# Performance work log

Hardware: AMD Instinct MI355X
Metric: run time of the kernel (lower is better)

## Reference

```python
import jax, jax.numpy as jnp
import numpy as np

N_NODES = 100000
N_EDGES = 1600000
IN_DIM, HID_DIM, OUT_DIM = 128, 64, 64
NEG_SLOPE = 0.2


def _gat_layer(h_in, src, dst, W, a_src, a_dst, b, n_nodes):
    # h: [N, F_out]
    h = h_in @ W.T
    alpha_src = h @ a_src  # [N]
    alpha_dst = h @ a_dst  # [N]
    # per-edge raw attention logits (edge j->i: src=j, dst=i)
    e = jax.nn.leaky_relu(alpha_src[src] + alpha_dst[dst], NEG_SLOPE)  # [E]
    # segment softmax over incoming edges of each dst node
    m = jax.ops.segment_max(e, dst, num_segments=n_nodes)
    ex = jnp.exp(e - m[dst])
    denom = jax.ops.segment_sum(ex, dst, num_segments=n_nodes)
    alpha = ex / denom[dst]  # [E], denom > 0 thanks to self-loops
    out = jax.ops.segment_sum(h[src] * alpha[:, None], dst, num_segments=n_nodes)
    return out + b


def setup_inputs() -> dict:
    key = jax.random.key(0)
    ks = jax.random.split(key, 12)
    x = jax.random.normal(ks[0], (N_NODES, IN_DIM), dtype=jnp.float32)
    edge_index = jax.random.randint(ks[1], (2, N_EDGES), 0, N_NODES)
    edge_attr = jax.random.normal(ks[2], (N_EDGES, 1), dtype=jnp.float32)
    s1 = 1.0 / np.sqrt(IN_DIM)
    s2 = 1.0 / np.sqrt(HID_DIM)
    W1 = jax.random.normal(ks[3], (HID_DIM, IN_DIM), dtype=jnp.float32) * s1
    att_src1 = jax.random.normal(ks[4], (HID_DIM,), dtype=jnp.float32) * s2
    att_dst1 = jax.random.normal(ks[5], (HID_DIM,), dtype=jnp.float32) * s2
    b1 = jnp.zeros((HID_DIM,), dtype=jnp.float32)
    W2 = jax.random.normal(ks[6], (OUT_DIM, HID_DIM), dtype=jnp.float32) * s2
    att_src2 = jax.random.normal(ks[7], (OUT_DIM,), dtype=jnp.float32) * s2
    att_dst2 = jax.random.normal(ks[8], (OUT_DIM,), dtype=jnp.float32) * s2
    b2 = jnp.zeros((OUT_DIM,), dtype=jnp.float32)
    return {"x": x, "edge_index": edge_index, "edge_attr": edge_attr,
            "W1": W1, "att_src1": att_src1, "att_dst1": att_dst1, "b1": b1,
            "W2": W2, "att_src2": att_src2, "att_dst2": att_dst2, "b2": b2}


def reference(x, edge_index, edge_attr, W1, att_src1, att_dst1, b1,
              W2, att_src2, att_dst2, b2):
    n = x.shape[0]
    # add self-loops (PyG GATConv default); edge_attr unused (edge_dim=None)
    loop = jnp.arange(n, dtype=edge_index.dtype)
    src = jnp.concatenate([edge_index[0], loop])
    dst = jnp.concatenate([edge_index[1], loop])
    h = _gat_layer(x, src, dst, W1, att_src1, att_dst1, b1, n)
    h = jax.nn.relu(h)
    h = _gat_layer(h, src, dst, W2, att_src2, att_dst2, b2, n)
    # global_mean_pool with batch=None -> mean over all nodes, shape [1, F]
    return jnp.mean(h, axis=0, keepdims=True)
```

## Files before the change

kernel.cpp:

```cpp
#include <hip/hip_runtime.h>

#define NEG_SLOPE 0.2f
#define BSHIFT 6
#define NBMAX 2048
#define BCAP 1408
#define CHUNK 4096

typedef __attribute__((ext_vector_type(8))) short short8;
typedef __attribute__((ext_vector_type(4))) float f32x4;

__device__ __forceinline__ unsigned short f2b(float x) {
    unsigned u = __float_as_uint(x);
    u += 0x7fff + ((u >> 16) & 1);
    return (unsigned short)(u >> 16);
}
__device__ __forceinline__ float b2f(unsigned short u) {
    return __uint_as_float((unsigned)u << 16);
}

__global__ __launch_bounds__(256) void hist_kernel(
    const int* __restrict__ ei, int* __restrict__ hist, int E, int NB)
{
    __shared__ int cnt[NBMAX];
    const int tid = threadIdx.x;
    for (int i = tid; i < NB; i += 256) cnt[i] = 0;
    __syncthreads();
    const int start = blockIdx.x * CHUNK;
    const int end = min(start + CHUNK, E);
    for (int i = start + tid; i < end; i += 256)
        atomicAdd(&cnt[ei[E + i] >> BSHIFT], 1);
    __syncthreads();
    for (int i = tid; i < NB; i += 256)
        hist[(size_t)blockIdx.x * NB + i] = cnt[i];
}

__global__ __launch_bounds__(256) void colscan_kernel(
    int* __restrict__ hist, int* __restrict__ btotal, int NB, int NBLK)
{
    const int b = blockIdx.x * 256 + threadIdx.x;
    if (b >= NB) return;
    int run = 0;
    int blk = 0;
    for (; blk + 8 <= NBLK; blk += 8) {
        int w[8];
        #pragma unroll
        for (int j = 0; j < 8; ++j) w[j] = hist[(size_t)(blk + j) * NB + b];
        #pragma unroll
        for (int j = 0; j < 8; ++j) {
            hist[(size_t)(blk + j) * NB + b] = run;
            run += w[j];
        }
    }
    for (; blk < NBLK; ++blk) {
        int w = hist[(size_t)blk * NB + b];
        hist[(size_t)blk * NB + b] = run;
        run += w;
    }
    btotal[b] = run;
}

__global__ __launch_bounds__(256) void scatter_kernel(
    const int* __restrict__ ei, const int* __restrict__ hist,
    int* __restrict__ binned, int E, int NB)
{
    __shared__ int base[NBMAX], cnt2[NBMAX];
    const int tid = threadIdx.x;
    for (int i = tid; i < NB; i += 256) {
        base[i] = hist[(size_t)blockIdx.x * NB + i];
        cnt2[i] = 0;
    }
    __syncthreads();
    const int start = blockIdx.x * CHUNK;
    const int end = min(start + CHUNK, E);
    for (int i = start + tid; i < end; i += 256) {
        int s = ei[i], d = ei[E + i];
        int b = d >> BSHIFT;
        int r = base[b] + atomicAdd(&cnt2[b], 1);
        if (r < BCAP) binned[(size_t)b * BCAP + r] = (s << BSHIFT) | (d & 63);
    }
}

__global__ __launch_bounds__(256) void bscan_kernel(
    const int* __restrict__ btotal, int* __restrict__ bbase, int NB)
{
    __shared__ int lds[256];
    const int t = threadIdx.x;
    int v[8]; int s = 0;
    #pragma unroll
    for (int j = 0; j < 8; ++j) {
        int i = t * 8 + j;
        v[j] = (i < NB) ? min(btotal[i], BCAP) : 0;
        s += v[j];
    }
    lds[t] = s;
    __syncthreads();
    #pragma unroll
    for (int off = 1; off < 256; off <<= 1) {
        int x = (t >= off) ? lds[t - off] : 0;
        __syncthreads();
        lds[t] += x;
        __syncthreads();
    }
    int excl = (t > 0) ? lds[t - 1] : 0;
    #pragma unroll
    for (int j = 0; j < 8; ++j) {
        int i = t * 8 + j;
        if (i < NB) { bbase[i] = excl + 64 * i; excl += v[j]; }
    }
}

__global__ __launch_bounds__(256) void bucket_csr_kernel(
    const int* __restrict__ binned, const int* __restrict__ btotal,
    const int* __restrict__ bbase, int* __restrict__ row_ptr,
    int* __restrict__ esrc, int N)
{
    __shared__ int ldeg[64];
    __shared__ int lcur[64];
    const int b = blockIdx.x;
    const int tid = threadIdx.x;
    const int node0 = b << BSHIFT;
    const int cnt = min(btotal[b], BCAP);
    const int base_e = bbase[b];
    const int* bp = binned + (size_t)b * BCAP;

    if (tid < 64) ldeg[tid] = (node0 + tid < N) ? 1 : 0;
    __syncthreads();
    for (int i = tid; i < cnt; i += 256)
        atomicAdd(&ldeg[bp[i] & 63], 1);
    __syncthreads();
    if (tid < 64) {
        int v = ldeg[tid];
        int inc = v;
        #pragma unroll
        for (int off = 1; off < 64; off <<= 1) {
            int t2 = __shfl_up(inc, off, 64);
            if (tid >= off) inc += t2;
        }
        int excl = inc - v;
        int node = node0 + tid;
        if (node <= N) row_ptr[node] = base_e + excl;
        if (node < N) {
            esrc[base_e + excl] = node;
            lcur[tid] = base_e + excl + 1;
        }
    }
    __syncthreads();
    for (int i = tid; i < cnt; i += 256) {
        int v = bp[i];
        int pos = atomicAdd(&lcur[v & 63], 1);
        esrc[pos] = v >> BSHIFT;
    }
}

template<int K, bool BF16IN>
__global__ __launch_bounds__(256) void gemm_attn_kernel(
    const void* __restrict__ in_v, const float* __restrict__ W,
    const float* __restrict__ a_src, const float* __restrict__ a_dst,
    unsigned short* __restrict__ hb, float* __restrict__ asrc,
    float* __restrict__ adst, int N)
{
    constexpr int LDK = K + 8;
    __shared__ unsigned short xb[64 * LDK];
    __shared__ unsigned short wb[64 * LDK];
    __shared__ float avs[64], avd[64];

    const int tid = threadIdx.x;
    const int node0 = blockIdx.x * 64;
    const int w = tid >> 6;
    const int lane = tid & 63;
    const int col = lane & 15;
    const int quad = lane >> 4;

    if (tid < 64) { avs[tid] = a_src[tid]; avd[tid] = a_dst[tid]; }

    for (int i = tid; i < 64 * (K / 4); i += 256) {
        int r = i / (K / 4), c = i % (K / 4);
        float4 v = *(const float4*)&W[(size_t)r * K + 4 * c];
        *(ushort4*)&wb[r * LDK + 4 * c] =
            make_ushort4(f2b(v.x), f2b(v.y), f2b(v.z), f2b(v.w));
    }
    if (BF16IN) {
        const unsigned short* in = (const unsigned short*)in_v;
        for (int i = tid; i < 64 * (K / 8); i += 256) {
            int r = i / (K / 8), c = i % (K / 8);
            int node = node0 + r;
            ulonglong2 v = (node < N)
                ? *(const ulonglong2*)&in[(size_t)node * K + 8 * c]
                : make_ulonglong2(0ull, 0ull);
            *(ulonglong2*)&xb[r * LDK + 8 * c] = v;
        }
    } else {
        const float* in = (const float*)in_v;
        for (int i = tid; i < 64 * (K / 4); i += 256) {
            int r = i / (K / 4), c = i % (K / 4);
            int node = node0 + r;
            float4 v = (node < N) ? *(const float4*)&in[(size_t)node * K + 4 * c]
                                  : make_float4(0.f, 0.f, 0.f, 0.f);
            *(ushort4*)&xb[r * LDK + 4 * c] =
                make_ushort4(f2b(v.x), f2b(v.y), f2b(v.z), f2b(v.w));
        }
    }
    __syncthreads();

    f32x4 acc[4] = {f32x4{0,0,0,0}, f32x4{0,0,0,0}, f32x4{0,0,0,0}, f32x4{0,0,0,0}};
    #pragma unroll
    for (int kc = 0; kc < K / 32; ++kc) {
        short8 a = *(const short8*)&xb[(16 * w + col) * LDK + kc * 32 + quad * 8];
        #pragma unroll
        for (int j = 0; j < 4; ++j) {
            short8 b = *(const short8*)&wb[(16 * j + col) * LDK + kc * 32 + quad * 8];
            acc[j] = __builtin_amdgcn_mfma_f32_16x16x32_bf16(a, b, acc[j], 0, 0, 0);
        }
    }

    #pragma unroll
    for (int r = 0; r < 4; ++r) {
        const int node = node0 + 16 * w + quad * 4 + r;
        const bool valid = node < N;
        float vs = 0.f, vd = 0.f;
        #pragma unroll
        for (int j = 0; j < 4; ++j) {
            float hv = acc[j][r];
            int f = 16 * j + col;
            if (valid) hb[(size_t)node * 64 + f] = f2b(hv);
            vs = fmaf(hv, avs[f], vs);
            vd = fmaf(hv, avd[f], vd);
        }
        #pragma unroll
        for (int off = 8; off >= 1; off >>= 1) {
            vs += __shfl_down(vs, off, 16);
            vd += __shfl_down(vd, off, 16);
        }
        if (col == 0 && valid) { asrc[node] = vs; adst[node] = vd; }
    }
}

__global__ __launch_bounds__(256) void aggregate_csr_kernel(
    const int* __restrict__ row_ptr, const int* __restrict__ esrc,
    const float* __restrict__ asrc, const float* __restrict__ adst,
    const unsigned short* __restrict__ hb, const float* __restrict__ bias,
    unsigned short* __restrict__ gb, int N, int do_relu)
{
    const int node = (int)((blockIdx.x * 256 + threadIdx.x) >> 4);
    const int lane = threadIdx.x & 15;
    if (node >= N) return;
    const int beg = row_ptr[node];
    const int end = row_ptr[node + 1];
    const float ad = adst[node];
    float a0 = 0.f, a1 = 0.f, a2 = 0.f, a3 = 0.f, wsum = 0.f;
    int p = beg;
    for (; p + 4 <= end; p += 4) {
        int s[4]; ushort4 r[4]; float l[4];
        #pragma unroll
        for (int j = 0; j < 4; ++j) s[j] = esrc[p + j];
        #pragma unroll
        for (int j = 0; j < 4; ++j)
            r[j] = *(const ushort4*)(hb + (size_t)s[j] * 64 + lane * 4);
        #pragma unroll
        for (int j = 0; j < 4; ++j) l[j] = asrc[s[j]] + ad;
        #pragma unroll
        for (int j = 0; j < 4; ++j) {
            float ll = (l[j] > 0.f) ? l[j] : NEG_SLOPE * l[j];
            float w = __expf(ll);
            wsum += w;
            a0 = fmaf(w, b2f(r[j].x), a0);
            a1 = fmaf(w, b2f(r[j].y), a1);
            a2 = fmaf(w, b2f(r[j].z), a2);
            a3 = fmaf(w, b2f(r[j].w), a3);
        }
    }
    for (; p < end; ++p) {
        int s = esrc[p];
        ushort4 r = *(const ushort4*)(hb + (size_t)s * 64 + lane * 4);
        float l = asrc[s] + ad;
        l = (l > 0.f) ? l : NEG_SLOPE * l;
        float w = __expf(l);
        wsum += w;
        a0 = fmaf(w, b2f(r.x), a0);
        a1 = fmaf(w, b2f(r.y), a1);
        a2 = fmaf(w, b2f(r.z), a2);
        a3 = fmaf(w, b2f(r.w), a3);
    }
    const float inv = 1.0f / wsum;
    float4 v = make_float4(a0 * inv, a1 * inv, a2 * inv, a3 * inv);
    if (bias) {
        v.x += bias[lane * 4 + 0]; v.y += bias[lane * 4 + 1];
        v.z += bias[lane * 4 + 2]; v.w += bias[lane * 4 + 3];
    }
    if (do_relu) {
        v.x = fmaxf(v.x, 0.f); v.y = fmaxf(v.y, 0.f);
        v.z = fmaxf(v.z, 0.f); v.w = fmaxf(v.w, 0.f);
    }
    *(ushort4*)&gb[(size_t)node * 64 + lane * 4] =
        make_ushort4(f2b(v.x), f2b(v.y), f2b(v.z), f2b(v.w));
}

__global__ __launch_bounds__(256) void pool_kernel(
    const unsigned short* __restrict__ gb, const float* __restrict__ b2,
    float* __restrict__ out, int N)
{
    __shared__ float red[256];
    const int f = threadIdx.x & 63;
    const int sub = threadIdx.x >> 6;
    float acc = 0.f;
    for (int n = blockIdx.x * 4 + sub; n < N; n += gridDim.x * 4)
        acc += b2f(gb[(size_t)n * 64 + f]);
    red[threadIdx.x] = acc;
    __syncthreads();
    if (threadIdx.x < 64) {
        float s = red[f] + red[64 + f] + red[128 + f] + red[192 + f];
        atomicAdd(out + f, s * (1.0f / (float)N));
        if (blockIdx.x == 0) atomicAdd(out + f, b2[f]);
    }
}

extern "C" void kernel_launch(void* const* d_in, const int* in_sizes, int n_in,
                              void* d_out, int out_size, void* d_ws, size_t ws_size,
                              hipStream_t stream) {
    const float* x   = (const float*)d_in[0];
    const int*   ei  = (const int*)d_in[1];
    const float* W1  = (const float*)d_in[3];
    const float* as1 = (const float*)d_in[4];
    const float* ad1 = (const float*)d_in[5];
    const float* b1  = (const float*)d_in[6];
    const float* W2  = (const float*)d_in[7];
    const float* as2 = (const float*)d_in[8];
    const float* ad2 = (const float*)d_in[9];
    const float* b2  = (const float*)d_in[10];
    float* out = (float*)d_out;

    const int N = in_sizes[0] / 128;
    const int E = in_sizes[1] / 2;
    const int Etot = E + N;
    const int NB = (N + 63) >> BSHIFT;
    const int NBLK = (E + CHUNK - 1) / CHUNK;

    auto align4 = [](size_t v) { return (v + 3) & ~(size_t)3; };
    float* ws    = (float*)d_ws;
    size_t off = 0;
    unsigned short* hb = (unsigned short*)(ws + off); off += align4((size_t)N * 32);
    unsigned short* gb = (unsigned short*)(ws + off); off += align4((size_t)N * 32);
    float* asrc  = ws + off; off += align4(N);
    float* adst  = ws + off; off += align4(N);
    int* row_ptr = (int*)(ws + off); off += align4(N + 1);
    int* btotal  = (int*)(ws + off); off += NBMAX;
    int* bbase   = (int*)(ws + off); off += NBMAX;
    int* hist    = (int*)(ws + off); off += align4((size_t)NBLK * NB);
    int* esrc    = (int*)(ws + off); off += align4(Etot);
    int* binned  = (int*)gb;

    const int gemm_blocks = (N + 63) / 64;
    const int agg_blocks  = (int)(((size_t)N * 16 + 255) / 256);

    hipMemsetAsync(out, 0, 64 * sizeof(float), stream);

    hist_kernel<<<NBLK, 256, 0, stream>>>(ei, hist, E, NB);
    colscan_kernel<<<(NB + 255) / 256, 256, 0, stream>>>(hist, btotal, NB, NBLK);
    scatter_kernel<<<NBLK, 256, 0, stream>>>(ei, hist, binned, E, NB);
    bscan_kernel<<<1, 256, 0, stream>>>(btotal, bbase, NB);
    bucket_csr_kernel<<<NB, 256, 0, stream>>>(binned, btotal, bbase, row_ptr, esrc, N);

    gemm_attn_kernel<128, false><<<gemm_blocks, 256, 0, stream>>>(
        x, W1, as1, ad1, hb, asrc, adst, N);
    aggregate_csr_kernel<<<agg_blocks, 256, 0, stream>>>(
        row_ptr, esrc, asrc, adst, hb, b1, gb, N, 1);

    gemm_attn_kernel<64, true><<<gemm_blocks, 256, 0, stream>>>(
        gb, W2, as2, ad2, hb, asrc, adst, N);
    aggregate_csr_kernel<<<agg_blocks, 256, 0, stream>>>(
        row_ptr, esrc, asrc, adst, hb, nullptr, gb, N, 0);

    pool_kernel<<<512, 256, 0, stream>>>(gb, b2, out, N);
}
```

Baseline: 301.8 us.

## Build CSR with global atomics and widen per-lane aggregation to 16 features

Replaces the bucketed histogram/scatter CSR construction with a per-node degree count using global atomics, a two-pass block scan, and a direct atomic-cursor scatter of source indices. It also drops the BCAP per-bucket truncation. Separately, the aggregation kernel now uses 4 lanes per node with 16 features each, loaded as two 16-byte vectors, instead of 16 lanes with 4 features. The CSR change trades shared-memory binning for contended global atomics and scattered writes. The aggregation change raises register use and lowers thread-level parallelism per node.

```diff
diff --git a/kernel.cpp b/kernel.cpp
--- a/kernel.cpp
+++ b/kernel.cpp
@@ -1,10 +1,6 @@
 #include <hip/hip_runtime.h>
 
 #define NEG_SLOPE 0.2f
-#define BSHIFT 6
-#define NBMAX 2048
-#define BCAP 1408
-#define CHUNK 4096
 
 typedef __attribute__((ext_vector_type(8))) short short8;
 typedef __attribute__((ext_vector_type(4))) float f32x4;
@@ -18,78 +14,27 @@
     return __uint_as_float((unsigned)u << 16);
 }
 
-__global__ __launch_bounds__(256) void hist_kernel(
-    const int* __restrict__ ei, int* __restrict__ hist, int E, int NB)
-{
-    __shared__ int cnt[NBMAX];
-    const int tid = threadIdx.x;
-    for (int i = tid; i < NB; i += 256) cnt[i] = 0;
-    __syncthreads();
-    const int start = blockIdx.x * CHUNK;
-    const int end = min(start + CHUNK, E);
-    for (int i = start + tid; i < end; i += 256)
-        atomicAdd(&cnt[ei[E + i] >> BSHIFT], 1);
-    __syncthreads();
-    for (int i = tid; i < NB; i += 256)
-        hist[(size_t)blockIdx.x * NB + i] = cnt[i];
-}
-
-__global__ __launch_bounds__(256) void colscan_kernel(
-    int* __restrict__ hist, int* __restrict__ btotal, int NB, int NBLK)
-{
-    const int b = blockIdx.x * 256 + threadIdx.x;
-    if (b >= NB) return;
-    int run = 0;
-    int blk = 0;
-    for (; blk + 8 <= NBLK; blk += 8) {
-        int w[8];
-        #pragma unroll
-        for (int j = 0; j < 8; ++j) w[j] = hist[(size_t)(blk + j) * NB + b];
-        #pragma unroll
-        for (int j = 0; j < 8; ++j) {
-            hist[(size_t)(blk + j) * NB + b] = run;
-            run += w[j];
-        }
-    }
-    for (; blk < NBLK; ++blk) {
-        int w = hist[(size_t)blk * NB + b];
-        hist[(size_t)blk * NB + b] = run;
-        run += w;
-    }
-    btotal[b] = run;
-}
-
-__global__ __launch_bounds__(256) void scatter_kernel(
-    const int* __restrict__ ei, const int* __restrict__ hist,
-    int* __restrict__ binned, int E, int NB)
-{
-    __shared__ int base[NBMAX], cnt2[NBMAX];
-    const int tid = threadIdx.x;
-    for (int i = tid; i < NB; i += 256) {
-        base[i] = hist[(size_t)blockIdx.x * NB + i];
-        cnt2[i] = 0;
-    }
-    __syncthreads();
-    const int start = blockIdx.x * CHUNK;
-    const int end = min(start + CHUNK, E);
-    for (int i = start + tid; i < end; i += 256) {
-        int s = ei[i], d = ei[E + i];
-        int b = d >> BSHIFT;
-        int r = base[b] + atomicAdd(&cnt2[b], 1);
-        if (r < BCAP) binned[(size_t)b * BCAP + r] = (s << BSHIFT) | (d & 63);
-    }
-}
-
-__global__ __launch_bounds__(256) void bscan_kernel(
-    const int* __restrict__ btotal, int* __restrict__ bbase, int NB)
+__global__ __launch_bounds__(256) void deg_kernel(
+    const int* __restrict__ ei, int* __restrict__ deg, int E)
+{
+    int i = blockIdx.x * 256 + threadIdx.x;
+    const int stride = gridDim.x * 256;
+    for (; i < E; i += stride)
+        atomicAdd(&deg[ei[E + i]], 1);
+}
+
+__global__ __launch_bounds__(256) void scan1_kernel(
+    const int* __restrict__ deg, int* __restrict__ row_ptr,
+    int* __restrict__ bsum, int N)
 {
     __shared__ int lds[256];
     const int t = threadIdx.x;
+    const int base = blockIdx.x * 2048 + t * 8;
     int v[8]; int s = 0;
     #pragma unroll
     for (int j = 0; j < 8; ++j) {
-        int i = t * 8 + j;
-        v[j] = (i < NB) ? min(btotal[i], BCAP) : 0;
+        int i = base + j;
+        v[j] = (i < N) ? deg[i] + 1 : 0;
         s += v[j];
     }
     lds[t] = s;
@@ -102,53 +47,48 @@
         __syncthreads();
     }
     int excl = (t > 0) ? lds[t - 1] : 0;
+    if (t == 255) bsum[blockIdx.x] = lds[255];
     #pragma unroll
     for (int j = 0; j < 8; ++j) {
-        int i = t * 8 + j;
-        if (i < NB) { bbase[i] = excl + 64 * i; excl += v[j]; }
-    }
-}
-
-__global__ __launch_bounds__(256) void bucket_csr_kernel(
-    const int* __restrict__ binned, const int* __restrict__ btotal,
-    const int* __restrict__ bbase, int* __restrict__ row_ptr,
-    int* __restrict__ esrc, int N)
-{
-    __shared__ int ldeg[64];
-    __shared__ int lcur[64];
-    const int b = blockIdx.x;
-    const int tid = threadIdx.x;
-    const int node0 = b << BSHIFT;
-    const int cnt = min(btotal[b], BCAP);
-    const int base_e = bbase[b];
-    const int* bp = binned + (size_t)b * BCAP;
-
-    if (tid < 64) ldeg[tid] = (node0 + tid < N) ? 1 : 0;
-    __syncthreads();
-    for (int i = tid; i < cnt; i += 256)
-        atomicAdd(&ldeg[bp[i] & 63], 1);
-    __syncthreads();
-    if (tid < 64) {
-        int v = ldeg[tid];
-        int inc = v;
-        #pragma unroll
-        for (int off = 1; off < 64; off <<= 1) {
-            int t2 = __shfl_up(inc, off, 64);
-            if (tid >= off) inc += t2;
-        }
-        int excl = inc - v;
-        int node = node0 + tid;
-        if (node <= N) row_ptr[node] = base_e + excl;
-        if (node < N) {
-            esrc[base_e + excl] = node;
-            lcur[tid] = base_e + excl + 1;
-        }
-    }
-    __syncthreads();
-    for (int i = tid; i < cnt; i += 256) {
-        int v = bp[i];
-        int pos = atomicAdd(&lcur[v & 63], 1);
-        esrc[pos] = v >> BSHIFT;
+        int i = base + j;
+        if (i < N) row_ptr[i] = excl;
+        excl += v[j];
+    }
+}
+
+__global__ __launch_bounds__(256) void scan2_kernel(
+    int* __restrict__ row_ptr, int* __restrict__ cursor,
+    int* __restrict__ esrc, const int* __restrict__ bsum, int N, int Etot)
+{
+    const int t = threadIdx.x;
+    const int blk = blockIdx.x;
+    int p = 0;
+    for (int j = 0; j < blk; ++j) p += bsum[j];
+    const int base = blk * 2048 + t * 8;
+    #pragma unroll
+    for (int j = 0; j < 8; ++j) {
+        int i = base + j;
+        if (i < N) {
+            int r = row_ptr[i] + p;
+            row_ptr[i] = r;
+            esrc[r] = i;
+            cursor[i] = r + 1;
+        }
+    }
+    if (blk == 0 && t == 0) row_ptr[N] = Etot;
+}
+
+__global__ __launch_bounds__(256) void scatter_direct_kernel(
+    const int* __restrict__ ei, int* __restrict__ cursor,
+    int* __restrict__ esrc, int E)
+{
+    int i = blockIdx.x * 256 + threadIdx.x;
+    const int stride = gridDim.x * 256;
+    for (; i < E; i += stride) {
+        int s = ei[i];
+        int d = ei[E + i];
+        int pos = atomicAdd(&cursor[d], 1);
+        esrc[pos] = s;
     }
 }
 
@@ -241,21 +181,30 @@
     const unsigned short* __restrict__ hb, const float* __restrict__ bias,
     unsigned short* __restrict__ gb, int N, int do_relu)
 {
-    const int node = (int)((blockIdx.x * 256 + threadIdx.x) >> 4);
-    const int lane = threadIdx.x & 15;
+    const int node = (int)((blockIdx.x * 256 + threadIdx.x) >> 2);
+    const int lane = threadIdx.x & 3;
     if (node >= N) return;
     const int beg = row_ptr[node];
     const int end = row_ptr[node + 1];
     const float ad = adst[node];
-    float a0 = 0.f, a1 = 0.f, a2 = 0.f, a3 = 0.f, wsum = 0.f;
+    const unsigned short* hbase = hb + lane * 16;
+
+    float acc[16];
+    #pragma unroll
+    for (int k = 0; k < 16; ++k) acc[k] = 0.f;
+    float wsum = 0.f;
+
     int p = beg;
     for (; p + 4 <= end; p += 4) {
-        int s[4]; ushort4 r[4]; float l[4];
+        int s[4]; short8 r0[4], r1[4]; float l[4];
         #pragma unroll
         for (int j = 0; j < 4; ++j) s[j] = esrc[p + j];
         #pragma unroll
-        for (int j = 0; j < 4; ++j)
-            r[j] = *(const ushort4*)(hb + (size_t)s[j] * 64 + lane * 4);
+        for (int j = 0; j < 4; ++j) {
+            const unsigned short* hp = hbase + (size_t)s[j] * 64;
+            r0[j] = *(const short8*)hp;
+            r1[j] = *(const short8*)(hp + 8);
+        }
         #pragma unroll
         for (int j = 0; j < 4; ++j) l[j] = asrc[s[j]] + ad;
         #pragma unroll
@@ -263,36 +212,45 @@
             float ll = (l[j] > 0.f) ? l[j] : NEG_SLOPE * l[j];
             float w = __expf(ll);
             wsum += w;
-            a0 = fmaf(w, b2f(r[j].x), a0);
-            a1 = fmaf(w, b2f(r[j].y), a1);
-            a2 = fmaf(w, b2f(r[j].z), a2);
-            a3 = fmaf(w, b2f(r[j].w), a3);
+            #pragma unroll
+            for (int k = 0; k < 8; ++k)
+                acc[k] = fmaf(w, b2f((unsigned short)r0[j][k]), acc[k]);
+            #pragma unroll
+            for (int k = 0; k < 8; ++k)
+                acc[8 + k] = fmaf(w, b2f((unsigned short)r1[j][k]), acc[8 + k]);
         }
     }
     for (; p < end; ++p) {
         int s = esrc[p];
-        ushort4 r = *(const ushort4*)(hb + (size_t)s * 64 + lane * 4);
+        const unsigned short* hp = hbase + (size_t)s * 64;
+        short8 r0 = *(const short8*)hp;
+        short8 r1 = *(const short8*)(hp + 8);
         float l = asrc[s] + ad;
         l = (l > 0.f) ? l : NEG_SLOPE * l;
         float w = __expf(l);
         wsum += w;
-        a0 = fmaf(w, b2f(r.x), a0);
-        a1 = fmaf(w, b2f(r.y), a1);
-        a2 = fmaf(w, b2f(r.z), a2);
-        a3 = fmaf(w, b2f(r.w), a3);
-    }
+        #pragma unroll
+        for (int k = 0; k < 8; ++k)
+            acc[k] = fmaf(w, b2f((unsigned short)r0[k]), acc[k]);
+        #pragma unroll
+        for (int k = 0; k < 8; ++k)
+            acc[8 + k] = fmaf(w, b2f((unsigned short)r1[k]), acc[8 + k]);
+    }
+
     const float inv = 1.0f / wsum;
-    float4 v = make_float4(a0 * inv, a1 * inv, a2 * inv, a3 * inv);
-    if (bias) {
-        v.x += bias[lane * 4 + 0]; v.y += bias[lane * 4 + 1];
-        v.z += bias[lane * 4 + 2]; v.w += bias[lane * 4 + 3];
-    }
-    if (do_relu) {
-        v.x = fmaxf(v.x, 0.f); v.y = fmaxf(v.y, 0.f);
-        v.z = fmaxf(v.z, 0.f); v.w = fmaxf(v.w, 0.f);
-    }
-    *(ushort4*)&gb[(size_t)node * 64 + lane * 4] =
-        make_ushort4(f2b(v.x), f2b(v.y), f2b(v.z), f2b(v.w));
+    short8 s0, s1;
+    #pragma unroll
+    for (int k = 0; k < 8; ++k) {
+        float v0 = acc[k] * inv;
+        float v1 = acc[8 + k] * inv;
+        if (bias) { v0 += bias[lane * 16 + k]; v1 += bias[lane * 16 + 8 + k]; }
+        if (do_relu) { v0 = fmaxf(v0, 0.f); v1 = fmaxf(v1, 0.f); }
+        s0[k] = (short)f2b(v0);
+        s1[k] = (short)f2b(v1);
+    }
+    unsigned short* gp = gb + (size_t)node * 64 + lane * 16;
+    *(short8*)gp = s0;
+    *(short8*)(gp + 8) = s1;
 }
 
 __global__ __launch_bounds__(256) void pool_kernel(
@@ -332,8 +290,6 @@
     const int N = in_sizes[0] / 128;
     const int E = in_sizes[1] / 2;
     const int Etot = E + N;
-    const int NB = (N + 63) >> BSHIFT;
-    const int NBLK = (E + CHUNK - 1) / CHUNK;
 
     auto align4 = [](size_t v) { return (v + 3) & ~(size_t)3; };
     float* ws    = (float*)d_ws;
@@ -343,22 +299,21 @@
     float* asrc  = ws + off; off += align4(N);
     float* adst  = ws + off; off += align4(N);
     int* row_ptr = (int*)(ws + off); off += align4(N + 1);
-    int* btotal  = (int*)(ws + off); off += NBMAX;
-    int* bbase   = (int*)(ws + off); off += NBMAX;
-    int* hist    = (int*)(ws + off); off += align4((size_t)NBLK * NB);
+    int* deg     = (int*)(ws + off); off += align4(N);
+    int* bsum    = (int*)(ws + off); off += 64;
     int* esrc    = (int*)(ws + off); off += align4(Etot);
-    int* binned  = (int*)gb;
 
     const int gemm_blocks = (N + 63) / 64;
-    const int agg_blocks  = (int)(((size_t)N * 16 + 255) / 256);
+    const int agg_blocks  = (int)(((size_t)N * 4 + 255) / 256);
+    const int NS1 = (N + 2047) / 2048;
 
     hipMemsetAsync(out, 0, 64 * sizeof(float), stream);
-
-    hist_kernel<<<NBLK, 256, 0, stream>>>(ei, hist, E, NB);
-    colscan_kernel<<<(NB + 255) / 256, 256, 0, stream>>>(hist, btotal, NB, NBLK);
-    scatter_kernel<<<NBLK, 256, 0, stream>>>(ei, hist, binned, E, NB);
-    bscan_kernel<<<1, 256, 0, stream>>>(btotal, bbase, NB);
-    bucket_csr_kernel<<<NB, 256, 0, stream>>>(binned, btotal, bbase, row_ptr, esrc, N);
+    hipMemsetAsync(deg, 0, (size_t)N * sizeof(int), stream);
+
+    deg_kernel<<<2048, 256, 0, stream>>>(ei, deg, E);
+    scan1_kernel<<<NS1, 256, 0, stream>>>(deg, row_ptr, bsum, N);
+    scan2_kernel<<<NS1, 256, 0, stream>>>(row_ptr, deg, esrc, bsum, N, Etot);
+    scatter_direct_kernel<<<2048, 256, 0, stream>>>(ei, deg, esrc, E);
 
     gemm_attn_kernel<128, false><<<gemm_blocks, 256, 0, stream>>>(
         x, W1, as1, ad1, hb, asrc, adst, N);
```

Result: slower. 448.4 us (+48.6%).

## Fuse final aggregation with mean pool, parallelize column scan, deepen gather unroll

Applied to the files above, without the earlier changes.

The second-layer aggregation now accumulates its normalized outputs straight into a shared-memory per-block sum and atomically adds to the pooled output. This removes the bf16 write of the final features and the separate pool kernel pass. The column scan uses one wavefront per bucket with a shuffle-based prefix scan instead of one serial thread per bucket. Scatter blocks are remapped to interleave chunk order, and the aggregation gather loop is unrolled to 8 edges to keep more loads in flight. The costs are more LDS atomics, higher register pressure from the deeper unroll, and a different float summation order in the pooled result.

```diff
diff --git a/kernel.cpp b/kernel.cpp
--- a/kernel.cpp
+++ b/kernel.cpp
@@ -37,26 +37,24 @@
 __global__ __launch_bounds__(256) void colscan_kernel(
     int* __restrict__ hist, int* __restrict__ btotal, int NB, int NBLK)
 {
-    const int b = blockIdx.x * 256 + threadIdx.x;
-    if (b >= NB) return;
+    const int col = (int)((blockIdx.x * 256 + threadIdx.x) >> 6);
+    const int ln  = threadIdx.x & 63;
+    if (col >= NB) return;
     int run = 0;
-    int blk = 0;
-    for (; blk + 8 <= NBLK; blk += 8) {
-        int w[8];
-        #pragma unroll
-        for (int j = 0; j < 8; ++j) w[j] = hist[(size_t)(blk + j) * NB + b];
-        #pragma unroll
-        for (int j = 0; j < 8; ++j) {
-            hist[(size_t)(blk + j) * NB + b] = run;
-            run += w[j];
-        }
-    }
-    for (; blk < NBLK; ++blk) {
-        int w = hist[(size_t)blk * NB + b];
-        hist[(size_t)blk * NB + b] = run;
-        run += w;
-    }
-    btotal[b] = run;
+    for (int r0 = 0; r0 < NBLK; r0 += 64) {
+        const int r = r0 + ln;
+        const bool ok = (r < NBLK);
+        int v = ok ? hist[(size_t)r * NB + col] : 0;
+        int inc = v;
+        #pragma unroll
+        for (int off = 1; off < 64; off <<= 1) {
+            int x = __shfl_up(inc, off, 64);
+            if (ln >= off) inc += x;
+        }
+        if (ok) hist[(size_t)r * NB + col] = run + inc - v;
+        run += __shfl(inc, 63, 64);
+    }
+    if (ln == 0) btotal[col] = run;
 }
 
 __global__ __launch_bounds__(256) void scatter_kernel(
@@ -64,13 +62,18 @@
     int* __restrict__ binned, int E, int NB)
 {
     __shared__ int base[NBMAX], cnt2[NBMAX];
+    const int nblk = gridDim.x;
+    const int q = nblk >> 3, rr = nblk & 7;
+    const int x = blockIdx.x & 7, k = blockIdx.x >> 3;
+    const int chunk = ((x < rr) ? x * (q + 1) : rr * (q + 1) + (x - rr) * q) + k;
+
     const int tid = threadIdx.x;
     for (int i = tid; i < NB; i += 256) {
-        base[i] = hist[(size_t)blockIdx.x * NB + i];
+        base[i] = hist[(size_t)chunk * NB + i];
         cnt2[i] = 0;
     }
     __syncthreads();
-    const int start = blockIdx.x * CHUNK;
+    const int start = chunk * CHUNK;
     const int end = min(start + CHUNK, E);
     for (int i = start + tid; i < end; i += 256) {
         int s = ei[i], d = ei[E + i];
@@ -249,17 +252,17 @@
     const float ad = adst[node];
     float a0 = 0.f, a1 = 0.f, a2 = 0.f, a3 = 0.f, wsum = 0.f;
     int p = beg;
-    for (; p + 4 <= end; p += 4) {
-        int s[4]; ushort4 r[4]; float l[4];
-        #pragma unroll
-        for (int j = 0; j < 4; ++j) s[j] = esrc[p + j];
-        #pragma unroll
-        for (int j = 0; j < 4; ++j)
+    for (; p + 8 <= end; p += 8) {
+        int s[8]; ushort4 r[8]; float l[8];
+        #pragma unroll
+        for (int j = 0; j < 8; ++j) s[j] = esrc[p + j];
+        #pragma unroll
+        for (int j = 0; j < 8; ++j)
             r[j] = *(const ushort4*)(hb + (size_t)s[j] * 64 + lane * 4);
         #pragma unroll
-        for (int j = 0; j < 4; ++j) l[j] = asrc[s[j]] + ad;
-        #pragma unroll
-        for (int j = 0; j < 4; ++j) {
+        for (int j = 0; j < 8; ++j) l[j] = asrc[s[j]] + ad;
+        #pragma unroll
+        for (int j = 0; j < 8; ++j) {
             float ll = (l[j] > 0.f) ? l[j] : NEG_SLOPE * l[j];
             float w = __expf(ll);
             wsum += w;
@@ -295,22 +298,70 @@
         make_ushort4(f2b(v.x), f2b(v.y), f2b(v.z), f2b(v.w));
 }
 
-__global__ __launch_bounds__(256) void pool_kernel(
-    const unsigned short* __restrict__ gb, const float* __restrict__ b2,
+__global__ __launch_bounds__(256) void aggregate_pool_kernel(
+    const int* __restrict__ row_ptr, const int* __restrict__ esrc,
+    const float* __restrict__ asrc, const float* __restrict__ adst,
+    const unsigned short* __restrict__ hb, const float* __restrict__ b2,
     float* __restrict__ out, int N)
 {
-    __shared__ float red[256];
-    const int f = threadIdx.x & 63;
-    const int sub = threadIdx.x >> 6;
-    float acc = 0.f;
-    for (int n = blockIdx.x * 4 + sub; n < N; n += gridDim.x * 4)
-        acc += b2f(gb[(size_t)n * 64 + f]);
-    red[threadIdx.x] = acc;
-    __syncthreads();
-    if (threadIdx.x < 64) {
-        float s = red[f] + red[64 + f] + red[128 + f] + red[192 + f];
-        atomicAdd(out + f, s * (1.0f / (float)N));
-        if (blockIdx.x == 0) atomicAdd(out + f, b2[f]);
+    __shared__ float red[64];
+    const int tid = threadIdx.x;
+    if (tid < 64) red[tid] = 0.f;
+    __syncthreads();
+
+    const int node = (int)((blockIdx.x * 256 + tid) >> 4);
+    const int lane = tid & 15;
+    const bool valid = node < N;
+    const int beg = valid ? row_ptr[node] : 0;
+    const int end = valid ? row_ptr[node + 1] : 0;
+    const float ad = valid ? adst[node] : 0.f;
+
+    float a0 = 0.f, a1 = 0.f, a2 = 0.f, a3 = 0.f, wsum = 0.f;
+    int p = beg;
+    for (; p + 8 <= end; p += 8) {
+        int s[8]; ushort4 r[8]; float l[8];
+        #pragma unroll
+        for (int j = 0; j < 8; ++j) s[j] = esrc[p + j];
+        #pragma unroll
+        for (int j = 0; j < 8; ++j)
+            r[j] = *(const ushort4*)(hb + (size_t)s[j] * 64 + lane * 4);
+        #pragma unroll
+        for (int j = 0; j < 8; ++j) l[j] = asrc[s[j]] + ad;
+        #pragma unroll
+        for (int j = 0; j < 8; ++j) {
+            float ll = (l[j] > 0.f) ? l[j] : NEG_SLOPE * l[j];
+            float w = __expf(ll);
+            wsum += w;
+            a0 = fmaf(w, b2f(r[j].x), a0);
+            a1 = fmaf(w, b2f(r[j].y), a1);
+            a2 = fmaf(w, b2f(r[j].z), a2);
+            a3 = fmaf(w, b2f(r[j].w), a3);
+        }
+    }
+    for (; p < end; ++p) {
+        int s = esrc[p];
+        ushort4 r = *(const ushort4*)(hb + (size_t)s * 64 + lane * 4);
+        float l = asrc[s] + ad;
+        l = (l > 0.f) ? l : NEG_SLOPE * l;
+        float w = __expf(l);
+        wsum += w;
+        a0 = fmaf(w, b2f(r.x), a0);
+        a1 = fmaf(w, b2f(r.y), a1);
+        a2 = fmaf(w, b2f(r.z), a2);
+        a3 = fmaf(w, b2f(r.w), a3);
+    }
+
+    if (valid) {
+        const float inv = 1.0f / wsum;
+        atomicAdd(&red[lane * 4 + 0], a0 * inv);
+        atomicAdd(&red[lane * 4 + 1], a1 * inv);
+        atomicAdd(&red[lane * 4 + 2], a2 * inv);
+        atomicAdd(&red[lane * 4 + 3], a3 * inv);
+    }
+    __syncthreads();
+    if (tid < 64) {
+        atomicAdd(out + tid, red[tid] * (1.0f / (float)N));
+        if (blockIdx.x == 0) atomicAdd(out + tid, b2[tid]);
     }
 }
 
@@ -355,7 +406,7 @@
     hipMemsetAsync(out, 0, 64 * sizeof(float), stream);
 
     hist_kernel<<<NBLK, 256, 0, stream>>>(ei, hist, E, NB);
-    colscan_kernel<<<(NB + 255) / 256, 256, 0, stream>>>(hist, btotal, NB, NBLK);
+    colscan_kernel<<<(NB * 64 + 255) / 256, 256, 0, stream>>>(hist, btotal, NB, NBLK);
     scatter_kernel<<<NBLK, 256, 0, stream>>>(ei, hist, binned, E, NB);
     bscan_kernel<<<1, 256, 0, stream>>>(btotal, bbase, NB);
     bucket_csr_kernel<<<NB, 256, 0, stream>>>(binned, btotal, bbase, row_ptr, esrc, N);
@@ -367,8 +418,6 @@
 
     gemm_attn_kernel<64, true><<<gemm_blocks, 256, 0, stream>>>(
         gb, W2, as2, ad2, hb, asrc, adst, N);
-    aggregate_csr_kernel<<<agg_blocks, 256, 0, stream>>>(
-        row_ptr, esrc, asrc, adst, hb, nullptr, gb, N, 0);
-
-    pool_kernel<<<512, 256, 0, stream>>>(gb, b2, out, N);
-}
+    aggregate_pool_kernel<<<agg_blocks, 256, 0, stream>>>(
+        row_ptr, esrc, asrc, adst, hb, b2, out, N);
+}
```

Result: slower. 396.8 us (+31.5%).
